# Kernel tuning notes

Hardware: AMD Instinct MI355X
Metric: run time of the kernel (lower is better)

The kernel has to match this reference:

```python
import jax, jax.numpy as jnp
import numpy as np

BN_EPS = 1e-5


def _bn_relu(h, gamma, beta):
    # BatchNorm1d in training mode: normalize over (batch, length) per channel
    mean = h.mean(axis=(0, 2), keepdims=True)
    var = h.var(axis=(0, 2), keepdims=True)
    h = (h - mean) * jax.lax.rsqrt(var + BN_EPS)
    h = h * gamma[None, :, None] + beta[None, :, None]
    return jax.nn.relu(h)


def _gather(ldesc, idx):
    # ldesc: [B, D, N], idx: [B, M] -> [B, D, M]
    B, D, N = ldesc.shape
    M = idx.shape[1]
    return jnp.take_along_axis(ldesc, jnp.broadcast_to(idx[:, None, :], (B, D, M)), axis=2)


def _scatter_mean(src, idx, N):
    # per-batch scatter-mean: src [B, D, M], idx [B, M] -> [B, D, N]
    def one(s, i):
        D = s.shape[0]
        sums = jnp.zeros((D, N), s.dtype).at[:, i].add(s)
        cnts = jnp.zeros((N,), s.dtype).at[i].add(1.0)
        return sums / jnp.maximum(cnts, 1.0)[None, :]
    return jax.vmap(one)(src, idx)


def _endpoint_update(ldesc, line_enc, idx, W1, b1, g1, bt1, W2, b2):
    B, D, _ = ldesc.shape
    ld = _gather(ldesc, idx)                                   # [B, D, 2L]
    # flip endpoint pairs: neighbor endpoint of each endpoint
    neigh = ld.reshape(B, D, -1, 2)[..., ::-1].reshape(B, D, -1)
    msg = jnp.concatenate([ld, neigh, line_enc], axis=1)       # [B, 3D, 2L]
    h = jnp.einsum('oc,bcm->bom', W1, msg) + b1[None, :, None]  # Conv1d k=1
    h = _bn_relu(h, g1, bt1)
    out = jnp.einsum('oc,bcm->bom', W2, h) + b2[None, :, None]
    return out                                                  # [B, D, 2L]


def setup_inputs() -> dict:
    key = jax.random.key(0)
    ks = jax.random.split(key, 12)
    B, D, N, M = 8, 256, 8192, 8192
    inp = {
        'ldesc0': jax.random.normal(ks[0], (B, D, N), jnp.float32),
        'ldesc1': jax.random.normal(ks[1], (B, D, N), jnp.float32),
        'line_enc0': jax.random.normal(ks[2], (B, D, M), jnp.float32),
        'line_enc1': jax.random.normal(ks[3], (B, D, M), jnp.float32),
        'lines_junc_idx0': jax.random.randint(ks[4], (B, M), 0, N),
        'lines_junc_idx1': jax.random.randint(ks[5], (B, M), 0, N),
        'W1': jax.random.normal(ks[6], (2 * D, 3 * D), jnp.float32) * (1.0 / np.sqrt(3 * D)),
        'b1': jnp.zeros((2 * D,), jnp.float32),
        'g1': jnp.ones((2 * D,), jnp.float32),
        'bt1': jnp.zeros((2 * D,), jnp.float32),
        'W2': jax.random.normal(ks[7], (D, 2 * D), jnp.float32) * (1.0 / np.sqrt(2 * D)),
        'b2': jnp.zeros((D,), jnp.float32),
    }
    return inp


def reference(ldesc0, ldesc1, line_enc0, line_enc1, lines_junc_idx0, lines_junc_idx1,
              W1, b1, g1, bt1, W2, b2):
    N = ldesc0.shape[2]
    up0 = _endpoint_update(ldesc0, line_enc0, lines_junc_idx0, W1, b1, g1, bt1, W2, b2)
    up1 = _endpoint_update(ldesc1, line_enc1, lines_junc_idx1, W1, b1, g1, bt1, W2, b2)
    out0 = ldesc0 + _scatter_mean(up0, lines_junc_idx0, N)
    out1 = ldesc1 + _scatter_mean(up1, lines_junc_idx1, N)
    return (out0, out1)
```

## Files before the change

kernel.cpp:

```cpp
#include <hip/hip_runtime.h>
#include <hip/hip_bf16.h>

#define B_  8
#define D_  256
#define N_  8192
#define M_  8192
#define O1_ 512
#define K1_ 768
#define K2_ 512

typedef unsigned short u16;
typedef __attribute__((ext_vector_type(8))) short bf8;
typedef __attribute__((ext_vector_type(4))) float f4;

static __device__ __forceinline__ float bf2f(u16 u) {
    unsigned v = ((unsigned)u) << 16;
    return __uint_as_float(v);
}
static __device__ __forceinline__ u16 f2bf(float f) {
    __hip_bfloat16 h = __float2bfloat16(f);
    return *reinterpret_cast<u16*>(&h);
}
static __device__ __forceinline__ void gl_lds16(const u16* g, u16* l) {
    __builtin_amdgcn_global_load_lds((const __attribute__((address_space(1))) void*)g,
                                     (__attribute__((address_space(3))) void*)l, 16, 0, 0);
}

__global__ __launch_bounds__(256) void k_transpose_bf16(const float* __restrict__ src,
                                                        u16* __restrict__ dst, int R, int C) {
    __shared__ float t[32][33];
    const int b  = blockIdx.z;
    const int c0 = blockIdx.x * 32, r0 = blockIdx.y * 32;
    const int tx = threadIdx.x, ty = threadIdx.y;
    const float* s = src + (size_t)b * R * C;
    u16* d = dst + (size_t)b * C * R;
#pragma unroll
    for (int i = 0; i < 4; ++i) {
        int r = r0 + ty + i * 8;
        t[ty + i * 8][tx] = s[(size_t)r * C + (c0 + tx)];
    }
    __syncthreads();
#pragma unroll
    for (int i = 0; i < 4; ++i) {
        int c = c0 + ty + i * 8;
        d[(size_t)c * R + (r0 + tx)] = f2bf(t[tx][ty + i * 8]);
    }
}

__global__ __launch_bounds__(256) void k_convert_w(const float* __restrict__ W1, const float* __restrict__ W2,
                                                   u16* __restrict__ W1b, u16* __restrict__ W2b) {
    int i = blockIdx.x * 256 + threadIdx.x;
    const int n1 = O1_ * K1_;
    const int n2 = D_ * K2_;
    if (i < n1) W1b[i] = f2bf(W1[i]);
    int j = i - n1;
    if (j >= 0 && j < n2) W2b[j] = f2bf(W2[j]);
}

__global__ __launch_bounds__(256) void k_gemm1(const u16* __restrict__ W1b,
                                               const u16* __restrict__ Tld,
                                               const u16* __restrict__ Tle,
                                               const int* __restrict__ idx,
                                               u16* __restrict__ hbuf) {
    __shared__ u16 At[128 * 32];
    __shared__ u16 Bt[128 * 32];
    const int b  = blockIdx.z;
    const int o0 = blockIdx.y * 128;
    const int m0 = blockIdx.x * 128;
    const int tid = threadIdx.x;
    const int w = tid >> 6, l = tid & 63;
    const int lr = l >> 2;
    const int lc = (l & 3) * 8;

    const u16* pA[2]; const u16* pB0[2]; const u16* pB1[2]; const u16* pB2[2];
#pragma unroll
    for (int t = 0; t < 2; ++t) {
        int row = t * 64 + w * 16 + lr;
        pA[t] = W1b + (size_t)(o0 + row) * K1_ + lc;
        int m  = m0 + row;
        int na = idx[b * M_ + m];
        int nb = idx[b * M_ + (m ^ 1)];
        pB0[t] = Tld + (size_t)(b * N_ + na) * D_ + lc;
        pB1[t] = Tld + (size_t)(b * N_ + nb) * D_ + lc;
        pB2[t] = Tle + (size_t)(b * M_ + m) * D_ + lc;
    }

    const int wr = w >> 1, wc = w & 1;
    f4 acc[4][4];
#pragma unroll
    for (int i = 0; i < 4; ++i)
#pragma unroll
        for (int j = 0; j < 4; ++j) acc[i][j] = {0.f, 0.f, 0.f, 0.f};

    const int aoff = (wr * 64 + (l & 15)) * 32 + (l >> 4) * 8;
    const int boff = (wc * 64 + (l & 15)) * 32 + (l >> 4) * 8;

    for (int kk = 0; kk < 24; ++kk) {
        const int seg  = kk >> 3;
        const int coff = (kk & 7) * 32;
#pragma unroll
        for (int t = 0; t < 2; ++t) {
            gl_lds16(pA[t] + kk * 32, At + (t * 64 + w * 16) * 32);
            const u16* src = (seg == 0) ? (pB0[t] + coff)
                           : (seg == 1) ? (pB1[t] + coff)
                                        : (pB2[t] + coff);
            gl_lds16(src, Bt + (t * 64 + w * 16) * 32);
        }
        __syncthreads();
        bf8 aF[4], bF[4];
#pragma unroll
        for (int i = 0; i < 4; ++i) aF[i] = *reinterpret_cast<const bf8*>(&At[aoff + i * 16 * 32]);
#pragma unroll
        for (int j = 0; j < 4; ++j) bF[j] = *reinterpret_cast<const bf8*>(&Bt[boff + j * 16 * 32]);
#pragma unroll
        for (int i = 0; i < 4; ++i)
#pragma unroll
            for (int j = 0; j < 4; ++j)
                acc[i][j] = __builtin_amdgcn_mfma_f32_16x16x32_bf16(aF[i], bF[j], acc[i][j], 0, 0, 0);
        __syncthreads();
    }

#pragma unroll
    for (int j = 0; j < 4; ++j) {
        int m = m0 + wc * 64 + j * 16 + (l & 15);
        size_t rowbase = (size_t)(b * M_ + m) * O1_;
#pragma unroll
        for (int i = 0; i < 4; ++i) {
            int orow = o0 + wr * 64 + i * 16 + (l >> 4) * 4;
            ushort4 pk;
            pk.x = f2bf(acc[i][j].x);
            pk.y = f2bf(acc[i][j].y);
            pk.z = f2bf(acc[i][j].z);
            pk.w = f2bf(acc[i][j].w);
            *reinterpret_cast<ushort4*>(&hbuf[rowbase + orow]) = pk;
        }
    }
}

__global__ __launch_bounds__(256) void k_stats(const u16* __restrict__ hbuf, float* __restrict__ stats) {
    const int t = threadIdx.x;
    const size_t row0 = (size_t)blockIdx.x * 256;
    float s0 = 0.f, q0 = 0.f, s1 = 0.f, q1 = 0.f;
    for (int r = 0; r < 256; ++r) {
        const u16* p = hbuf + (row0 + r) * O1_;
        float v0 = bf2f(p[t]);
        float v1 = bf2f(p[t + 256]);
        s0 += v0; q0 += v0 * v0;
        s1 += v1; q1 += v1 * v1;
    }
    atomicAdd(&stats[t], s0);
    atomicAdd(&stats[O1_ + t], q0);
    atomicAdd(&stats[t + 256], s1);
    atomicAdd(&stats[O1_ + t + 256], q1);
}

__global__ void k_finalize_ac(const float* __restrict__ stats, const float* __restrict__ g1,
                              const float* __restrict__ bt1, float* __restrict__ ac) {
    int o = blockIdx.x * 256 + threadIdx.x;
    if (o >= O1_) return;
    const float inv = 1.0f / ((float)B_ * (float)M_);
    float mean = stats[o] * inv;
    float var  = stats[O1_ + o] * inv - mean * mean;
    var = fmaxf(var, 0.0f);
    float a = g1[o] * rsqrtf(var + 1e-5f);
    ac[o] = a;
    ac[O1_ + o] = bt1[o] - mean * a;
}

__global__ void k_count_int(const int* __restrict__ idx, int* __restrict__ cnt) {
    int i = blockIdx.x * 256 + threadIdx.x;
    if (i < B_ * M_) atomicAdd(&cnt[(i >> 13) * N_ + idx[i]], 1);
}

__global__ __launch_bounds__(1024) void k_scan(const int* __restrict__ cnt, int* __restrict__ offs,
                                               int* __restrict__ fill) {
    __shared__ int wsum[1024];
    const int b = blockIdx.x;
    const int t = threadIdx.x;
    const int base = b * N_;
    int v[8]; int s = 0;
#pragma unroll
    for (int k = 0; k < 8; ++k) { v[k] = cnt[base + t * 8 + k]; s += v[k]; }
    wsum[t] = s;
    __syncthreads();
    for (int off = 1; off < 1024; off <<= 1) {
        int add = (t >= off) ? wsum[t - off] : 0;
        __syncthreads();
        wsum[t] += add;
        __syncthreads();
    }
    int run = (t > 0) ? wsum[t - 1] : 0;
#pragma unroll
    for (int k = 0; k < 8; ++k) {
        offs[base + t * 8 + k] = run;
        fill[base + t * 8 + k] = run;
        run += v[k];
    }
}

__global__ void k_fill(const int* __restrict__ idx, int* __restrict__ fill, int* __restrict__ mlist) {
    int i = blockIdx.x * 256 + threadIdx.x;
    if (i < B_ * M_) {
        int b = i >> 13, m = i & (M_ - 1);
        int pos = atomicAdd(&fill[b * N_ + idx[i]], 1);
        mlist[(size_t)b * M_ + pos] = m;
    }
}

__global__ __launch_bounds__(256) void k_gemm2(const u16* __restrict__ W2b,
                                               const u16* __restrict__ hbuf,
                                               const float* __restrict__ ac,
                                               const float* __restrict__ b2,
                                               u16* __restrict__ up) {
    __shared__ u16 At[128 * 32];
    __shared__ u16 Bt[128 * 32];
    __shared__ float acs[1024];
    const int b  = blockIdx.z;
    const int d0 = blockIdx.y * 128;
    const int m0 = blockIdx.x * 128;
    const int tid = threadIdx.x;
    const int w = tid >> 6, l = tid & 63;
    const int lr = l >> 2, lc = (l & 3) * 8;

    acs[tid]       = ac[tid];
    acs[tid + 256] = ac[tid + 256];
    acs[tid + 512] = ac[tid + 512];
    acs[tid + 768] = ac[tid + 768];

    const u16* pA[2]; const u16* pB[2];
#pragma unroll
    for (int t = 0; t < 2; ++t) {
        int row = t * 64 + w * 16 + lr;
        pA[t] = W2b + (size_t)(d0 + row) * K2_ + lc;
        int m  = m0 + row;
        pB[t] = hbuf + (size_t)(b * M_ + m) * O1_ + lc;
    }
    const int wr = w >> 1, wc = w & 1;
    f4 acc[4][4];
#pragma unroll
    for (int i = 0; i < 4; ++i)
#pragma unroll
        for (int j = 0; j < 4; ++j) acc[i][j] = {0.f, 0.f, 0.f, 0.f};

    const int aoff = (wr * 64 + (l & 15)) * 32 + (l >> 4) * 8;
    const int boff = (wc * 64 + (l & 15)) * 32 + (l >> 4) * 8;
    const int bdst = (w * 16 + lr) * 32 + lc;

    __syncthreads();

    for (int kk = 0; kk < 16; ++kk) {
        const int o = kk * 32 + lc;
        f4 A0 = *reinterpret_cast<const f4*>(&acs[o]);
        f4 A1 = *reinterpret_cast<const f4*>(&acs[o + 4]);
        f4 C0 = *reinterpret_cast<const f4*>(&acs[512 + o]);
        f4 C1 = *reinterpret_cast<const f4*>(&acs[512 + o + 4]);
#pragma unroll
        for (int t = 0; t < 2; ++t) {
            gl_lds16(pA[t] + kk * 32, At + (t * 64 + w * 16) * 32);
            const ushort4* ps = reinterpret_cast<const ushort4*>(pB[t] + kk * 32);
            ushort4 v0 = ps[0], v1 = ps[1];
            union { ushort4 u4[2]; bf8 v8; } pk;
            pk.u4[0].x = f2bf(fmaxf(bf2f(v0.x) * A0.x + C0.x, 0.0f));
            pk.u4[0].y = f2bf(fmaxf(bf2f(v0.y) * A0.y + C0.y, 0.0f));
            pk.u4[0].z = f2bf(fmaxf(bf2f(v0.z) * A0.z + C0.z, 0.0f));
            pk.u4[0].w = f2bf(fmaxf(bf2f(v0.w) * A0.w + C0.w, 0.0f));
            pk.u4[1].x = f2bf(fmaxf(bf2f(v1.x) * A1.x + C1.x, 0.0f));
            pk.u4[1].y = f2bf(fmaxf(bf2f(v1.y) * A1.y + C1.y, 0.0f));
            pk.u4[1].z = f2bf(fmaxf(bf2f(v1.z) * A1.z + C1.z, 0.0f));
            pk.u4[1].w = f2bf(fmaxf(bf2f(v1.w) * A1.w + C1.w, 0.0f));
            *reinterpret_cast<bf8*>(&Bt[t * 64 * 32 + bdst]) = pk.v8;
        }
        __syncthreads();
        bf8 aF[4], bF[4];
#pragma unroll
        for (int i = 0; i < 4; ++i) aF[i] = *reinterpret_cast<const bf8*>(&At[aoff + i * 16 * 32]);
#pragma unroll
        for (int j = 0; j < 4; ++j) bF[j] = *reinterpret_cast<const bf8*>(&Bt[boff + j * 16 * 32]);
#pragma unroll
        for (int i = 0; i < 4; ++i)
#pragma unroll
            for (int j = 0; j < 4; ++j)
                acc[i][j] = __builtin_amdgcn_mfma_f32_16x16x32_bf16(aF[i], bF[j], acc[i][j], 0, 0, 0);
        __syncthreads();
    }

#pragma unroll
    for (int j = 0; j < 4; ++j) {
        int m = m0 + wc * 64 + j * 16 + (l & 15);
        size_t rowbase = (size_t)(b * M_ + m) * D_;
#pragma unroll
        for (int i = 0; i < 4; ++i) {
            int d = d0 + wr * 64 + i * 16 + (l >> 4) * 4;
            ushort4 pk;
            pk.x = f2bf(acc[i][j].x + b2[d + 0]);
            pk.y = f2bf(acc[i][j].y + b2[d + 1]);
            pk.z = f2bf(acc[i][j].z + b2[d + 2]);
            pk.w = f2bf(acc[i][j].w + b2[d + 3]);
            *reinterpret_cast<ushort4*>(&up[rowbase + d]) = pk;
        }
    }
}

__global__ __launch_bounds__(256) void k_reduce_finalize(const float* __restrict__ ldesc,
                                                         const u16* __restrict__ up,
                                                         const int* __restrict__ cnt,
                                                         const int* __restrict__ offs,
                                                         const int* __restrict__ mlist,
                                                         float* __restrict__ out) {
    __shared__ float lds[32][257];
    const int b  = blockIdx.z;
    const int n0 = blockIdx.x * 32;
    const int tx = threadIdx.x, ty = threadIdx.y;
#pragma unroll
    for (int i = 0; i < 4; ++i) {
        int nl = ty + i * 8;
        int n  = n0 + nl;
        int c   = cnt[b * N_ + n];
        int off = offs[b * N_ + n];
        float inv = 1.0f / (float)max(c, 1);
        float acc[8] = {0.f, 0.f, 0.f, 0.f, 0.f, 0.f, 0.f, 0.f};
        for (int e = 0; e < c; ++e) {
            int m = mlist[(size_t)b * M_ + off + e];
            const ushort4* row = reinterpret_cast<const ushort4*>(up + (size_t)(b * M_ + m) * D_ + tx * 8);
            ushort4 aa = row[0], bb = row[1];
            acc[0] += bf2f(aa.x); acc[1] += bf2f(aa.y); acc[2] += bf2f(aa.z); acc[3] += bf2f(aa.w);
            acc[4] += bf2f(bb.x); acc[5] += bf2f(bb.y); acc[6] += bf2f(bb.z); acc[7] += bf2f(bb.w);
        }
#pragma unroll
        for (int k = 0; k < 8; ++k) lds[nl][tx * 8 + k] = acc[k] * inv;
    }
    __syncthreads();
#pragma unroll
    for (int i = 0; i < 32; ++i) {
        int d = ty + i * 8;
        size_t o2 = (size_t)(b * D_ + d) * N_ + n0 + tx;
        out[o2] = ldesc[o2] + lds[tx][d];
    }
}

__global__ void k_marker(float* out, float v) { out[0] = v; }

extern "C" void kernel_launch(void* const* d_in, const int* in_sizes, int n_in,
                              void* d_out, int out_size, void* d_ws, size_t ws_size,
                              hipStream_t stream) {
    const float* ldesc0 = (const float*)d_in[0];
    const float* ldesc1 = (const float*)d_in[1];
    const float* le0    = (const float*)d_in[2];
    const float* le1    = (const float*)d_in[3];
    const int*   idx0   = (const int*)d_in[4];
    const int*   idx1   = (const int*)d_in[5];
    const float* W1     = (const float*)d_in[6];
    const float* g1     = (const float*)d_in[8];
    const float* bt1    = (const float*)d_in[9];
    const float* W2     = (const float*)d_in[10];
    const float* b2     = (const float*)d_in[11];
    float* out = (float*)d_out;

    char* ws = (char*)d_ws;
    const size_t oTld   = 0;
    const size_t oTle   = 33554432;
    const size_t oH     = 67108864;
    const size_t oW1b   = 134217728;
    const size_t oW2b   = oW1b + 786432;
    const size_t oStats = oW2b + 262144;
    const size_t oAC    = oStats + 4096;
    const size_t NEED   = oAC + 4096;
    if (ws_size < NEED) {
        k_marker<<<1, 1, 0, stream>>>(out, 1000.0f + (float)(ws_size >> 20));
        return;
    }
    u16*   Tld   = (u16*)(ws + oTld);
    u16*   up    = (u16*)(ws + oTld);
    u16*   Tle   = (u16*)(ws + oTle);
    int*   cnt   = (int*)(ws + oTle);
    int*   offs  = (int*)(ws + oTle + 262144);
    int*   fill  = (int*)(ws + oTle + 524288);
    int*   mlist = (int*)(ws + oTle + 786432);
    u16*   hbuf  = (u16*)(ws + oH);
    u16*   W1b   = (u16*)(ws + oW1b);
    u16*   W2b   = (u16*)(ws + oW2b);
    float* stats = (float*)(ws + oStats);
    float* ac    = (float*)(ws + oAC);

    k_convert_w<<<2048, 256, 0, stream>>>(W1, W2, W1b, W2b);

    const dim3 tb(32, 8);
    for (int s = 0; s < 2; ++s) {
        const float* ld  = s ? ldesc1 : ldesc0;
        const float* le  = s ? le1 : le0;
        const int*   idx = s ? idx1 : idx0;
        float* outp = out + (size_t)s * B_ * D_ * N_;

        k_transpose_bf16<<<dim3(N_ / 32, D_ / 32, B_), tb, 0, stream>>>(ld, Tld, D_, N_);
        k_transpose_bf16<<<dim3(M_ / 32, D_ / 32, B_), tb, 0, stream>>>(le, Tle, D_, M_);
        k_gemm1<<<dim3(M_ / 128, O1_ / 128, B_), 256, 0, stream>>>(W1b, Tld, Tle, idx, hbuf);
        hipMemsetAsync(stats, 0, 4096, stream);
        k_stats<<<256, 256, 0, stream>>>(hbuf, stats);
        k_finalize_ac<<<2, 256, 0, stream>>>(stats, g1, bt1, ac);
        hipMemsetAsync(cnt, 0, (size_t)B_ * N_ * 4, stream);
        k_count_int<<<B_ * M_ / 256, 256, 0, stream>>>(idx, cnt);
        k_scan<<<B_, 1024, 0, stream>>>(cnt, offs, fill);
        k_fill<<<B_ * M_ / 256, 256, 0, stream>>>(idx, fill, mlist);
        k_gemm2<<<dim3(M_ / 128, D_ / 128, B_), 256, 0, stream>>>(W2b, hbuf, ac, b2, up);
        k_reduce_finalize<<<dim3(N_ / 32, 1, B_), tb, 0, stream>>>(ld, up, cnt, offs, mlist, outp);
    }
}
```

Before: 476.3 us.

## Rewrite gather-GEMM1 with 256x256 tiles, 4-stage LDS pipeline and swizzle

Rewrites the first gathered GEMM to use 512-thread blocks computing 256x256 output tiles, with a 4-buffer shared-memory ring fed by async global-to-LDS loads, so loads for later k-steps overlap the MFMA work. It adds an XOR swizzle on LDS rows to cut bank conflicts, uses explicit vmcnt waits and one barrier per k-step instead of two, and raises wave priority around the MFMA block. The larger tile improves operand reuse but uses far more LDS (128KB per block) and more accumulator registers, which may limit occupancy.

```diff
diff --git a/kernel.cpp b/kernel.cpp
--- a/kernel.cpp
+++ b/kernel.cpp
@@ -24,6 +24,9 @@
 static __device__ __forceinline__ void gl_lds16(const u16* g, u16* l) {
     __builtin_amdgcn_global_load_lds((const __attribute__((address_space(1))) void*)g,
                                      (__attribute__((address_space(3))) void*)l, 16, 0, 0);
+}
+static __device__ __forceinline__ int swz64(int r) {
+    return (((r >> 1) & 1) << 4) | (((r >> 2) & 1) << 5);
 }
 
 __global__ __launch_bounds__(256) void k_transpose_bf16(const float* __restrict__ src,
@@ -57,76 +60,115 @@
     if (j >= 0 && j < n2) W2b[j] = f2bf(W2[j]);
 }
 
-__global__ __launch_bounds__(256) void k_gemm1(const u16* __restrict__ W1b,
-                                               const u16* __restrict__ Tld,
-                                               const u16* __restrict__ Tle,
-                                               const int* __restrict__ idx,
-                                               u16* __restrict__ hbuf) {
-    __shared__ u16 At[128 * 32];
-    __shared__ u16 Bt[128 * 32];
+#define NT1 24
+__global__ __launch_bounds__(512, 2) void k_gemm1(const u16* __restrict__ W1b,
+                                                  const u16* __restrict__ Tld,
+                                                  const u16* __restrict__ Tle,
+                                                  const int* __restrict__ idx,
+                                                  u16* __restrict__ hbuf) {
+    __shared__ u16 LA[4][256 * 32];
+    __shared__ u16 LB[4][256 * 32];
     const int b  = blockIdx.z;
-    const int o0 = blockIdx.y * 128;
-    const int m0 = blockIdx.x * 128;
+    const int o0 = blockIdx.y * 256;
+    const int m0 = blockIdx.x * 256;
     const int tid = threadIdx.x;
     const int w = tid >> 6, l = tid & 63;
-    const int lr = l >> 2;
-    const int lc = (l & 3) * 8;
-
-    const u16* pA[2]; const u16* pB0[2]; const u16* pB1[2]; const u16* pB2[2];
-#pragma unroll
-    for (int t = 0; t < 2; ++t) {
-        int row = t * 64 + w * 16 + lr;
-        pA[t] = W1b + (size_t)(o0 + row) * K1_ + lc;
-        int m  = m0 + row;
-        int na = idx[b * M_ + m];
-        int nb = idx[b * M_ + (m ^ 1)];
-        pB0[t] = Tld + (size_t)(b * N_ + na) * D_ + lc;
-        pB1[t] = Tld + (size_t)(b * N_ + nb) * D_ + lc;
-        pB2[t] = Tle + (size_t)(b * M_ + m) * D_ + lc;
-    }
-
-    const int wr = w >> 1, wc = w & 1;
-    f4 acc[4][4];
-#pragma unroll
-    for (int i = 0; i < 4; ++i)
+    const int wr = w >> 2;
+    const int wcn = w & 3;
+
+    const int srow   = tid >> 2;
+    const int scol16 = (tid & 3) * 16;
+
+    int na[2], nb[2], mrow[2];
+    const u16* aSrc[2];
+    int bcol[2];
+#pragma unroll
+    for (int j = 0; j < 2; ++j) {
+        int r = srow + j * 128;
+        int m = m0 + r;
+        mrow[j] = m;
+        na[j] = idx[b * M_ + m];
+        nb[j] = idx[b * M_ + (m ^ 1)];
+        int sw = swz64(r);
+        aSrc[j] = W1b + (size_t)(o0 + r) * K1_ + ((scol16 ^ sw) >> 1);
+        bcol[j] = (scol16 ^ sw) >> 1;
+    }
+
+    int ar[8], br[4];
+#pragma unroll
+    for (int i = 0; i < 8; ++i) {
+        int r = wr * 128 + i * 16 + (l & 15);
+        ar[i] = r * 32 + ((((l >> 4) * 16) ^ swz64(r)) >> 1);
+    }
+#pragma unroll
+    for (int j = 0; j < 4; ++j) {
+        int r = wcn * 64 + j * 16 + (l & 15);
+        br[j] = r * 32 + ((((l >> 4) * 16) ^ swz64(r)) >> 1);
+    }
+
+#define STAGE1(kt, buf)                                                              \
+    {                                                                                \
+        const int seg = (kt) >> 3;                                                   \
+        const int off = ((kt) & 7) * 32;                                             \
+        _Pragma("unroll")                                                            \
+        for (int j = 0; j < 2; ++j)                                                  \
+            gl_lds16(aSrc[j] + (kt) * 32, &LA[buf][j * 4096 + tid * 8]);             \
+        _Pragma("unroll")                                                            \
+        for (int j = 0; j < 2; ++j) {                                                \
+            const u16* s;                                                            \
+            if (seg == 0)      s = Tld + (size_t)(b * N_ + na[j]) * D_ + off + bcol[j]; \
+            else if (seg == 1) s = Tld + (size_t)(b * N_ + nb[j]) * D_ + off + bcol[j]; \
+            else               s = Tle + (size_t)(b * M_ + mrow[j]) * D_ + off + bcol[j]; \
+            gl_lds16(s, &LB[buf][j * 4096 + tid * 8]);                               \
+        }                                                                            \
+    }
+
+    f4 acc[8][4];
+#pragma unroll
+    for (int i = 0; i < 8; ++i)
 #pragma unroll
         for (int j = 0; j < 4; ++j) acc[i][j] = {0.f, 0.f, 0.f, 0.f};
 
-    const int aoff = (wr * 64 + (l & 15)) * 32 + (l >> 4) * 8;
-    const int boff = (wc * 64 + (l & 15)) * 32 + (l >> 4) * 8;
-
-    for (int kk = 0; kk < 24; ++kk) {
-        const int seg  = kk >> 3;
-        const int coff = (kk & 7) * 32;
-#pragma unroll
-        for (int t = 0; t < 2; ++t) {
-            gl_lds16(pA[t] + kk * 32, At + (t * 64 + w * 16) * 32);
-            const u16* src = (seg == 0) ? (pB0[t] + coff)
-                           : (seg == 1) ? (pB1[t] + coff)
-                                        : (pB2[t] + coff);
-            gl_lds16(src, Bt + (t * 64 + w * 16) * 32);
-        }
-        __syncthreads();
-        bf8 aF[4], bF[4];
-#pragma unroll
-        for (int i = 0; i < 4; ++i) aF[i] = *reinterpret_cast<const bf8*>(&At[aoff + i * 16 * 32]);
-#pragma unroll
-        for (int j = 0; j < 4; ++j) bF[j] = *reinterpret_cast<const bf8*>(&Bt[boff + j * 16 * 32]);
-#pragma unroll
-        for (int i = 0; i < 4; ++i)
+    STAGE1(0, 0);
+    STAGE1(1, 1);
+    STAGE1(2, 2);
+    asm volatile("s_waitcnt vmcnt(8)" ::: "memory");
+    __builtin_amdgcn_s_barrier();
+    __builtin_amdgcn_sched_barrier(0);
+
+    for (int t = 0; t < NT1; ++t) {
+        const int buf = t & 3;
+        if (t + 3 < NT1) STAGE1(t + 3, (t + 3) & 3);
+
+        bf8 aF[8], bF[4];
+#pragma unroll
+        for (int i = 0; i < 8; ++i) aF[i] = *reinterpret_cast<const bf8*>(&LA[buf][ar[i]]);
+#pragma unroll
+        for (int j = 0; j < 4; ++j) bF[j] = *reinterpret_cast<const bf8*>(&LB[buf][br[j]]);
+
+        __builtin_amdgcn_s_setprio(1);
+#pragma unroll
+        for (int i = 0; i < 8; ++i)
 #pragma unroll
             for (int j = 0; j < 4; ++j)
                 acc[i][j] = __builtin_amdgcn_mfma_f32_16x16x32_bf16(aF[i], bF[j], acc[i][j], 0, 0, 0);
-        __syncthreads();
-    }
+        __builtin_amdgcn_s_setprio(0);
+
+        if (t <= NT1 - 4)      asm volatile("s_waitcnt vmcnt(8)" ::: "memory");
+        else if (t == NT1 - 3) asm volatile("s_waitcnt vmcnt(4)" ::: "memory");
+        else                   asm volatile("s_waitcnt vmcnt(0)" ::: "memory");
+        __builtin_amdgcn_s_barrier();
+        __builtin_amdgcn_sched_barrier(0);
+    }
+#undef STAGE1
 
 #pragma unroll
     for (int j = 0; j < 4; ++j) {
-        int m = m0 + wc * 64 + j * 16 + (l & 15);
+        int m = m0 + wcn * 64 + j * 16 + (l & 15);
         size_t rowbase = (size_t)(b * M_ + m) * O1_;
 #pragma unroll
-        for (int i = 0; i < 4; ++i) {
-            int orow = o0 + wr * 64 + i * 16 + (l >> 4) * 4;
+        for (int i = 0; i < 8; ++i) {
+            int orow = o0 + wr * 128 + i * 16 + (l >> 4) * 4;
             ushort4 pk;
             pk.x = f2bf(acc[i][j].x);
             pk.y = f2bf(acc[i][j].y);
@@ -393,7 +435,7 @@
 
         k_transpose_bf16<<<dim3(N_ / 32, D_ / 32, B_), tb, 0, stream>>>(ld, Tld, D_, N_);
         k_transpose_bf16<<<dim3(M_ / 32, D_ / 32, B_), tb, 0, stream>>>(le, Tle, D_, M_);
-        k_gemm1<<<dim3(M_ / 128, O1_ / 128, B_), 256, 0, stream>>>(W1b, Tld, Tle, idx, hbuf);
+        k_gemm1<<<dim3(M_ / 256, O1_ / 256, B_), 512, 0, stream>>>(W1b, Tld, Tle, idx, hbuf);
         hipMemsetAsync(stats, 0, 4096, stream);
         k_stats<<<256, 256, 0, stream>>>(hbuf, stats);
         k_finalize_ac<<<2, 256, 0, stream>>>(stats, g1, bt1, ac);
```

Result: no change. 485.0 us (+1.8%).
